# Performance work log

Hardware: AMD Instinct MI355X
Metric: run time of the kernel (lower is better)

The kernel has to match this reference:

```python
import jax, jax.numpy as jnp
import numpy as np

B, LQ, LK, DQ, DK, DV = 8, 2048, 2048, 1024, 1024, 1024
TOP_K = 64
NEG_INF = float('-inf')


def setup_inputs() -> dict:
    key = jax.random.key(0)
    kq, kk, kv, km, kw = jax.random.split(key, 5)
    queries = jax.random.normal(kq, (B, LQ, DQ), dtype=jnp.float32)
    keys = jax.random.normal(kk, (B, LK, DK), dtype=jnp.float32)
    values = jax.random.normal(kv, (B, LK, DV), dtype=jnp.float32)
    mask = jax.random.randint(km, (B, LQ, LK), 0, 2, dtype=jnp.int32)
    # nn.Linear(query_dim, key_dim, bias=False) weight: [key_dim, query_dim]
    W = jax.random.normal(kw, (DK, DQ), dtype=jnp.float32) / np.sqrt(DQ)
    return {"queries": queries, "keys": keys, "values": values,
            "mask": mask, "W": W, "top_k": TOP_K}


def reference(queries, keys, values, mask, W, top_k):
    # scores = (queries @ W.T) @ keys^T  -> [B, LQ, LK]  (method='general')
    q_proj = jnp.einsum('bqd,kd->bqk', queries, W)  # [B, LQ, DK]
    scores = jnp.einsum('bqd,btd->bqt', q_proj, keys)  # [B, LQ, LK]
    scores = jnp.where(mask == 0, NEG_INF, scores)
    alphas = jax.nn.softmax(scores, axis=-1)
    alphas = jnp.where(jnp.isnan(alphas), 0.0, alphas)  # fully-masked rows -> 0
    # top-k: zero out non-top-k probabilities, then re-softmax over the
    # resulting tensor (zeros contribute exp(0)=1, matching torch semantics)
    _, idx = jax.lax.top_k(alphas, top_k)  # [B, LQ, top_k]
    b_idx = jnp.arange(alphas.shape[0])[:, None, None]
    q_idx = jnp.arange(alphas.shape[1])[None, :, None]
    topk_mask = jnp.zeros(alphas.shape, alphas.dtype).at[b_idx, q_idx, idx].set(1.0)
    alphas = jnp.where(topk_mask == 0, 0.0, alphas)
    alphas = jax.nn.softmax(alphas, axis=-1)
    alphas = jnp.where(jnp.isnan(alphas), 0.0, alphas)
    # dropout_rate = 0.0 -> identity
    return jnp.einsum('bqt,btd->bqd', alphas, values)  # [B, LQ, DV]
```

## Files before the change

kernel.cpp:

```cpp
#include <hip/hip_runtime.h>
#include <math.h>

#define BATCH 8
#define SEQ   2048
#define DIM   1024
#define TOPK  64
#define NEGMASK -1e30f
#define CAND_THRESH 16.0f

typedef _Float16 f16;
typedef _Float16 f16x8 __attribute__((ext_vector_type(8)));
typedef float f32x4 __attribute__((ext_vector_type(4)));

__device__ __forceinline__ void async_load16(const void* g, void* l) {
  __builtin_amdgcn_global_load_lds(
      (const __attribute__((address_space(1))) void*)g,
      (__attribute__((address_space(3))) void*)l, 16, 0, 0);
}

__global__ __launch_bounds__(256) void colsum_partial_kernel(
    const float* __restrict__ values, float* __restrict__ partial) {
  int bid = blockIdx.x;
  int tc = bid >> 5;
  int b  = (bid >> 2) & 7;
  int dg = bid & 3;
  int d  = dg * 256 + threadIdx.x;
  const float* vp = values + ((size_t)b * SEQ + (size_t)tc * 256) * DIM + d;
  float s = 0.f;
  #pragma unroll 8
  for (int t = 0; t < 256; ++t) s += vp[(size_t)t * DIM];
  partial[((size_t)tc * BATCH + b) * DIM + d] = s;
}

__global__ __launch_bounds__(256) void colsum_reduce_kernel(
    const float* __restrict__ partial, float* __restrict__ colsum) {
  int idx = blockIdx.x * 256 + threadIdx.x;
  float s = 0.f;
  #pragma unroll
  for (int tc = 0; tc < 8; ++tc) s += partial[(size_t)tc * 8192 + idx];
  colsum[idx] = s;
}

__global__ __launch_bounds__(256) void cvt_f32_to_f16(
    const float* __restrict__ in, f16* __restrict__ out, int n) {
  int i = (blockIdx.x * 256 + threadIdx.x) * 4;
  if (i >= n) return;
  float4 v = *(const float4*)(in + i);
  union { f16 h[4]; uint2 u; } pk;
  pk.h[0] = (f16)v.x; pk.h[1] = (f16)v.y; pk.h[2] = (f16)v.z; pk.h[3] = (f16)v.w;
  *(uint2*)(out + i) = pk.u;
}


#define GEMM_PROLOGUE(APTR, BPTR)                                           \
  const int tid = threadIdx.x;                                              \
  const int wave = tid >> 6, lane = tid & 63;                               \
  const int wm = (wave >> 1) * 64, wn = (wave & 1) * 64;                    \
  const int r0 = wave * 32 + (lane >> 2);                                   \
  const int c16 = (lane & 3) ^ ((r0 >> 1) & 3);                            \
  const f16* srcA0 = (APTR) + (size_t)(m0 + r0) * DIM + c16 * 8;           \
  const f16* srcA1 = (APTR) + (size_t)(m0 + r0 + 16) * DIM + c16 * 8;      \
  const f16* srcB0 = (BPTR) + (size_t)(n0 + r0) * DIM + c16 * 8;           \
  const f16* srcB1 = (BPTR) + (size_t)(n0 + r0 + 16) * DIM + c16 * 8;      \
  char* ldsA0 = smA + wave * 2048;                                          \
  char* ldsA1 = smA + wave * 2048 + 1024;                                   \
  char* ldsB0 = smB + wave * 2048;                                          \
  char* ldsB1 = smB + wave * 2048 + 1024;                                   \
  int offA[4], offB[4];                                                     \
  _Pragma("unroll")                                                         \
  for (int i = 0; i < 4; ++i) {                                             \
    int r = wm + i * 16 + (lane & 15);                                      \
    offA[i] = r * 64 + ((lane >> 4) ^ ((r >> 1) & 3)) * 16;                 \
    int rn = wn + i * 16 + (lane & 15);                                     \
    offB[i] = rn * 64 + ((lane >> 4) ^ ((rn >> 1) & 3)) * 16;               \
  }                                                                         \
  f32x4 acc[4][4];                                                          \
  _Pragma("unroll")                                                         \
  for (int i = 0; i < 4; ++i)                                               \
    _Pragma("unroll")                                                       \
    for (int j = 0; j < 4; ++j)                                             \
      acc[i][j] = (f32x4){0.f, 0.f, 0.f, 0.f};                              \
  for (int k0 = 0; k0 < DIM; k0 += 32) {                                    \
    async_load16(srcA0 + k0, ldsA0);                                        \
    async_load16(srcA1 + k0, ldsA1);                                        \
    async_load16(srcB0 + k0, ldsB0);                                        \
    async_load16(srcB1 + k0, ldsB1);                                        \
    __syncthreads();                                                        \
    f16x8 af[4], bf[4];                                                     \
    _Pragma("unroll")                                                       \
    for (int i = 0; i < 4; ++i) {                                           \
      af[i] = *(const f16x8*)(smA + offA[i]);                               \
      bf[i] = *(const f16x8*)(smB + offB[i]);                               \
    }                                                                       \
    _Pragma("unroll")                                                       \
    for (int i = 0; i < 4; ++i)                                             \
      _Pragma("unroll")                                                     \
      for (int j = 0; j < 4; ++j)                                           \
        acc[i][j] = __builtin_amdgcn_mfma_f32_16x16x32_f16(                 \
            af[i], bf[j], acc[i][j], 0, 0, 0);                              \
    __syncthreads();                                                        \
  }

__global__ __launch_bounds__(256) void gemm_qproj(
    const f16* __restrict__ A, const f16* __restrict__ Bw,
    f16* __restrict__ C) {
  __shared__ __align__(128) char smA[8192];
  __shared__ __align__(128) char smB[8192];
  const int m0 = blockIdx.y * 128;
  const int n0 = blockIdx.x * 128;
  GEMM_PROLOGUE(A, Bw)
  const int cr = m0 + wm + (lane >> 4) * 4;
  const int cc = n0 + wn + (lane & 15);
  #pragma unroll
  for (int i = 0; i < 4; ++i)
    #pragma unroll
    for (int j = 0; j < 4; ++j)
      #pragma unroll
      for (int reg = 0; reg < 4; ++reg)
        C[(size_t)(cr + i * 16 + reg) * DIM + cc + j * 16] = (f16)acc[i][j][reg];
}

__global__ __launch_bounds__(256) void gemm_scores(
    const f16* __restrict__ QP, const f16* __restrict__ K16,
    const int* __restrict__ mask, float* __restrict__ S) {
  __shared__ __align__(128) char smA[8192];
  __shared__ __align__(128) char smB[8192];
  const int m0 = blockIdx.y * 128;
  const int n0 = blockIdx.x * 128;
  const int b  = m0 >> 11;
  const f16* Bk = K16 + (size_t)b * SEQ * DIM;
  GEMM_PROLOGUE(QP, Bk)
  const int cr = m0 + wm + (lane >> 4) * 4;
  const int cc = n0 + wn + (lane & 15);
  #pragma unroll
  for (int i = 0; i < 4; ++i)
    #pragma unroll
    for (int j = 0; j < 4; ++j)
      #pragma unroll
      for (int reg = 0; reg < 4; ++reg) {
        size_t off = (size_t)(cr + i * 16 + reg) * SEQ + cc + j * 16;
        S[off] = mask[off] ? acc[i][j][reg] : NEGMASK;
      }
}

__global__ __launch_bounds__(512) void topk_kernel(
    const float* __restrict__ scores_ws,
    const float* __restrict__ values,
    const float* __restrict__ colsum,
    float* __restrict__ out)
{
  __shared__ int   cidx[8][128];
  __shared__ float csc[8][128];
  const int wave = threadIdx.x >> 6;
  const int lane = threadIdx.x & 63;
  const int grow = blockIdx.x * 8 + wave;
  const int b    = grow >> 11;
  const float* srow = scores_ws + (size_t)grow * SEQ;
  int*   myidx = cidx[wave];
  float* mysc  = csc[wave];

  f32x4 s4[8];
  #pragma unroll
  for (int i = 0; i < 8; ++i)
    s4[i] = *(const f32x4*)(srow + i * 256 + lane * 4);

  float mv = -3e38f;
  #pragma unroll
  for (int i = 0; i < 8; ++i)
    #pragma unroll
    for (int j = 0; j < 4; ++j) mv = fmaxf(mv, s4[i][j]);
  #pragma unroll
  for (int off = 32; off > 0; off >>= 1) mv = fmaxf(mv, __shfl_xor(mv, off));
  const bool dead = (mv <= -1e29f);

  float Z = 1.f;
  if (!dead) {
    float zs = 0.f;
    #pragma unroll
    for (int i = 0; i < 8; ++i)
      #pragma unroll
      for (int j = 0; j < 4; ++j) zs += __expf(s4[i][j] - mv);
    #pragma unroll
    for (int off = 32; off > 0; off >>= 1) zs += __shfl_xor(zs, off);
    Z = zs;
  }
  const float invZ = 1.0f / Z;

  int cnt = 0;
  if (!dead) {
    const float thresh = mv - CAND_THRESH;
    const unsigned long long lmlt = (1ull << lane) - 1ull;
    #pragma unroll
    for (int i = 0; i < 8; ++i)
      #pragma unroll
      for (int j = 0; j < 4; ++j) {
        bool c = s4[i][j] > thresh;
        unsigned long long m = __ballot(c);
        if (c) {
          int pos = cnt + __popcll(m & lmlt);
          if (pos < 128) { myidx[pos] = i * 256 + lane * 4 + j; mysc[pos] = s4[i][j]; }
        }
        cnt += __popcll(m);
      }
  }
  asm volatile("s_waitcnt lgkmcnt(0)" ::: "memory");

  float total_g = 0.f;
  f32x4 oacc[4];
  #pragma unroll
  for (int j = 0; j < 4; ++j) oacc[j] = (f32x4){0.f, 0.f, 0.f, 0.f};
  const float* vbase = values + (size_t)b * SEQ * DIM;

  if (cnt <= 64) {
    for (int c = 0; c < cnt; ++c) {
      float g = expm1f(__expf(mysc[c] - mv) * invZ);
      total_g += g;
      const float* vrow = vbase + (size_t)myidx[c] * DIM;
      #pragma unroll
      for (int j = 0; j < 4; ++j) {
        f32x4 v = *(const f32x4*)(vrow + j * 256 + lane * 4);
        #pragma unroll
        for (int e = 0; e < 4; ++e) oacc[j][e] = fmaf(g, v[e], oacc[j][e]);
      }
    }
  } else {
    int nlist = cnt < 128 ? cnt : 128;
    for (int itk = 0; itk < TOPK; ++itk) {
      float bv = -3e38f; int bi = 1 << 30; int bsl = -1;
      #pragma unroll
      for (int h = 0; h < 2; ++h) {
        int sl = lane + h * 64;
        if (sl < nlist) {
          float v = mysc[sl]; int id = myidx[sl];
          if (v > bv || (v == bv && id < bi)) { bv = v; bi = id; bsl = sl; }
        }
      }
      #pragma unroll
      for (int off = 32; off > 0; off >>= 1) {
        float ov = __shfl_xor(bv, off);
        int   oi = __shfl_xor(bi, off);
        int   os = __shfl_xor(bsl, off);
        if (ov > bv || (ov == bv && oi < bi)) { bv = ov; bi = oi; bsl = os; }
      }
      if (bv <= -1e29f) break;
      float g = expm1f(__expf(bv - mv) * invZ);
      total_g += g;
      const float* vrow = vbase + (size_t)bi * DIM;
      #pragma unroll
      for (int j = 0; j < 4; ++j) {
        f32x4 v = *(const f32x4*)(vrow + j * 256 + lane * 4);
        #pragma unroll
        for (int e = 0; e < 4; ++e) oacc[j][e] = fmaf(g, v[e], oacc[j][e]);
      }
      if (lane == 0) mysc[bsl] = -3e38f;
      asm volatile("s_waitcnt lgkmcnt(0)" ::: "memory");
    }
  }

  const float inv = 1.0f / (2048.0f + total_g);
  const float* cs = colsum + (size_t)b * DIM;
  float* orow = out + (size_t)grow * DIM;
  #pragma unroll
  for (int j = 0; j < 4; ++j) {
    f32x4 c = *(const f32x4*)(cs + j * 256 + lane * 4);
    f32x4 o;
    #pragma unroll
    for (int e = 0; e < 4; ++e) o[e] = (c[e] + oacc[j][e]) * inv;
    *(f32x4*)(orow + j * 256 + lane * 4) = o;
  }
}

extern "C" void kernel_launch(void* const* d_in, const int* in_sizes, int n_in,
                              void* d_out, int out_size, void* d_ws, size_t ws_size,
                              hipStream_t stream) {
  const float* queries = (const float*)d_in[0];
  const float* keys    = (const float*)d_in[1];
  const float* values  = (const float*)d_in[2];
  const int*   mask    = (const int*)d_in[3];
  const float* W       = (const float*)d_in[4];
  float* out = (float*)d_out;

  char* base = (char*)d_ws;
  float* scores  = (float*)base;
  f16*   q16     = (f16*)base;
  f16*   w16     = (f16*)(base + (size_t)32 * 1024 * 1024);
  f16*   qp16    = (f16*)(base + (size_t)128 * 1024 * 1024);
  f16*   k16     = (f16*)(base + (size_t)160 * 1024 * 1024);
  float* colsum  = (float*)(base + (size_t)192 * 1024 * 1024);
  float* partial = colsum + 8192;

  colsum_partial_kernel<<<256, 256, 0, stream>>>(values, partial);
  colsum_reduce_kernel<<<32, 256, 0, stream>>>(partial, colsum);
  cvt_f32_to_f16<<<16384, 256, 0, stream>>>(queries, q16, 16384 * 1024);
  cvt_f32_to_f16<<<1024, 256, 0, stream>>>(W, w16, 1024 * 1024);
  gemm_qproj<<<dim3(8, 128), 256, 0, stream>>>(q16, w16, qp16);
  cvt_f32_to_f16<<<16384, 256, 0, stream>>>(keys, k16, 16384 * 1024);
  gemm_scores<<<dim3(16, 128), 256, 0, stream>>>(qp16, k16, mask, scores);
  topk_kernel<<<2048, 512, 0, stream>>>(scores, values, colsum, out);
}
```

Before: 321.8 us.

## Filter top-k candidates in score GEMM epilogue and bit-pack mask

A new kernel packs the int32 mask into 64-bit bitmasks. The score GEMM epilogue then applies the mask, takes a per-row max over each 128-column tile, and writes only scores within a threshold of that max into capped per-segment candidate slots, plus a count per segment. The top-k kernel reads these compact lists instead of full score rows, and builds the softmax denominator from candidates only. This removes the full fp32 score write and re-read and shrinks mask traffic inside the GEMM. In exchange it adds a mask-packing pass and a shared-memory sync in the epilogue, and it becomes approximate: scores below the threshold are dropped from Z, and segments with more than 28 candidates are truncated.

Result: slower. 366.4 us (+13.9%).

```diff
diff --git a/kernel.cpp b/kernel.cpp
--- a/kernel.cpp
+++ b/kernel.cpp
@@ -7,6 +7,7 @@
 #define TOPK  64
 #define NEGMASK -1e30f
 #define CAND_THRESH 16.0f
+#define CAP 28
 
 typedef _Float16 f16;
 typedef _Float16 f16x8 __attribute__((ext_vector_type(8)));
@@ -16,6 +17,16 @@
   __builtin_amdgcn_global_load_lds(
       (const __attribute__((address_space(1))) void*)g,
       (__attribute__((address_space(3))) void*)l, 16, 0, 0);
+}
+
+__global__ __launch_bounds__(256) void pack_mask_kernel(
+    const int* __restrict__ mask, unsigned long long* __restrict__ mb) {
+  const int wave = threadIdx.x >> 6, lane = threadIdx.x & 63;
+  for (size_t w = blockIdx.x * 4 + wave; w < (size_t)16384 * 32; w += 2048 * 4) {
+    int m = mask[w * 64 + lane];
+    unsigned long long bits = __ballot(m != 0);
+    if (lane == 0) mb[w] = bits;
+  }
 }
 
 __global__ __launch_bounds__(256) void colsum_partial_kernel(
@@ -122,7 +133,9 @@
 
 __global__ __launch_bounds__(256) void gemm_scores(
     const f16* __restrict__ QP, const f16* __restrict__ K16,
-    const int* __restrict__ mask, float* __restrict__ S) {
+    const unsigned long long* __restrict__ maskbits,
+    float2* __restrict__ cand,
+    int* __restrict__ counts) {
   __shared__ __align__(128) char smA[8192];
   __shared__ __align__(128) char smB[8192];
   const int m0 = blockIdx.y * 128;
@@ -130,130 +143,168 @@
   const int b  = m0 >> 11;
   const f16* Bk = K16 + (size_t)b * SEQ * DIM;
   GEMM_PROLOGUE(QP, Bk)
-  const int cr = m0 + wm + (lane >> 4) * 4;
-  const int cc = n0 + wn + (lane & 15);
+
+  const int g  = lane >> 4;
+  const int lc = lane & 15;
+  const int word = (n0 >> 6) + (wn >> 6);
+
   #pragma unroll
   for (int i = 0; i < 4; ++i)
     #pragma unroll
-    for (int j = 0; j < 4; ++j)
+    for (int reg = 0; reg < 4; ++reg) {
+      const int r = wm + i * 16 + g * 4 + reg;
+      const unsigned long long mw = maskbits[(size_t)(m0 + r) * 32 + word];
       #pragma unroll
-      for (int reg = 0; reg < 4; ++reg) {
-        size_t off = (size_t)(cr + i * 16 + reg) * SEQ + cc + j * 16;
-        S[off] = mask[off] ? acc[i][j][reg] : NEGMASK;
+      for (int j = 0; j < 4; ++j)
+        if (!((mw >> (lc + j * 16)) & 1ull)) acc[i][j][reg] = NEGMASK;
+    }
+
+  float* hm = (float*)smA;
+  #pragma unroll
+  for (int i = 0; i < 4; ++i)
+    #pragma unroll
+    for (int reg = 0; reg < 4; ++reg) {
+      const int r = wm + i * 16 + g * 4 + reg;
+      float m4 = fmaxf(fmaxf(acc[i][0][reg], acc[i][1][reg]),
+                       fmaxf(acc[i][2][reg], acc[i][3][reg]));
+      #pragma unroll
+      for (int off = 8; off >= 1; off >>= 1) m4 = fmaxf(m4, __shfl_xor(m4, off));
+      if (lc == 0) hm[r * 2 + (wn >> 6)] = m4;
+    }
+  __syncthreads();
+
+  const int pairbase = (n0 >> 7) * 2 + (wn >> 6);
+  #pragma unroll
+  for (int i = 0; i < 4; ++i)
+    #pragma unroll
+    for (int reg = 0; reg < 4; ++reg) {
+      const int r = wm + i * 16 + g * 4 + reg;
+      const float tm = fmaxf(hm[r * 2], hm[r * 2 + 1]);
+      const float thresh = fmaxf(tm - CAND_THRESH, -1e29f);
+      float2* slot = cand + ((size_t)(m0 + r) * 32 + pairbase) * CAP;
+      int cnt = 0;
+      #pragma unroll
+      for (int j = 0; j < 4; ++j) {
+        const float s = acc[i][j][reg];
+        const bool c = s > thresh;
+        const unsigned long long bal = __ballot(c);
+        const int seg = (int)((bal >> (g * 16)) & 0xFFFFull);
+        const int pos = cnt + __popc(seg & ((1 << lc) - 1));
+        if (c && pos < CAP) {
+          float2 e; e.x = s; e.y = __int_as_float(n0 + wn + j * 16 + lc);
+          slot[pos] = e;
+        }
+        cnt += __popc(seg);
       }
+      if (lc == 0) counts[(size_t)(m0 + r) * 32 + pairbase] = cnt < CAP ? cnt : CAP;
+    }
 }
 
 __global__ __launch_bounds__(512) void topk_kernel(
-    const float* __restrict__ scores_ws,
-    const float* __restrict__ values,
-    const float* __restrict__ colsum,
+    const float2* __restrict__ cand,
+    const int*    __restrict__ counts,
+    const float*  __restrict__ values,
+    const float*  __restrict__ colsum,
     float* __restrict__ out)
 {
-  __shared__ int   cidx[8][128];
-  __shared__ float csc[8][128];
+  __shared__ float ssc[8][128];
+  __shared__ int   sidx[8][128];
   const int wave = threadIdx.x >> 6;
   const int lane = threadIdx.x & 63;
   const int grow = blockIdx.x * 8 + wave;
   const int b    = grow >> 11;
-  const float* srow = scores_ws + (size_t)grow * SEQ;
-  int*   myidx = cidx[wave];
-  float* mysc  = csc[wave];
-
-  f32x4 s4[8];
-  #pragma unroll
-  for (int i = 0; i < 8; ++i)
-    s4[i] = *(const f32x4*)(srow + i * 256 + lane * 4);
+  float* msc = ssc[wave];
+  int*   mix = sidx[wave];
+
+  int cnt_p = 0;
+  if (lane < 32) cnt_p = counts[(size_t)grow * 32 + lane];
+  const float2* myslots = cand + ((size_t)grow * 32 + lane) * CAP;
 
   float mv = -3e38f;
-  #pragma unroll
-  for (int i = 0; i < 8; ++i)
-    #pragma unroll
-    for (int j = 0; j < 4; ++j) mv = fmaxf(mv, s4[i][j]);
+  for (int k = 0; k < cnt_p; ++k) mv = fmaxf(mv, myslots[k].x);
   #pragma unroll
   for (int off = 32; off > 0; off >>= 1) mv = fmaxf(mv, __shfl_xor(mv, off));
   const bool dead = (mv <= -1e29f);
 
-  float Z = 1.f;
-  if (!dead) {
-    float zs = 0.f;
-    #pragma unroll
-    for (int i = 0; i < 8; ++i)
-      #pragma unroll
-      for (int j = 0; j < 4; ++j) zs += __expf(s4[i][j] - mv);
-    #pragma unroll
-    for (int off = 32; off > 0; off >>= 1) zs += __shfl_xor(zs, off);
-    Z = zs;
-  }
-  const float invZ = 1.0f / Z;
-
-  int cnt = 0;
+  float total_g = 0.f;
+  f32x4 oacc[4];
+  #pragma unroll
+  for (int j = 0; j < 4; ++j) oacc[j] = (f32x4){0.f, 0.f, 0.f, 0.f};
+  const float* vbase = values + (size_t)b * SEQ * DIM;
+
   if (!dead) {
     const float thresh = mv - CAND_THRESH;
-    const unsigned long long lmlt = (1ull << lane) - 1ull;
-    #pragma unroll
-    for (int i = 0; i < 8; ++i)
-      #pragma unroll
-      for (int j = 0; j < 4; ++j) {
-        bool c = s4[i][j] > thresh;
-        unsigned long long m = __ballot(c);
-        if (c) {
-          int pos = cnt + __popcll(m & lmlt);
-          if (pos < 128) { myidx[pos] = i * 256 + lane * 4 + j; mysc[pos] = s4[i][j]; }
-        }
-        cnt += __popcll(m);
+    int f = 0; float zp = 0.f;
+    for (int k = 0; k < cnt_p; ++k) {
+      float s = myslots[k].x;
+      if (s > thresh) { ++f; zp += __expf(s - mv); }
+    }
+    int incl = f;
+    #pragma unroll
+    for (int off = 1; off < 64; off <<= 1) {
+      int t = __shfl_up(incl, off);
+      if (lane >= off) incl += t;
+    }
+    const int base = incl - f;
+    const int F = __shfl(incl, 63);
+    #pragma unroll
+    for (int off = 32; off > 0; off >>= 1) zp += __shfl_xor(zp, off);
+    const float Z = zp;
+    int w = 0;
+    for (int k = 0; k < cnt_p; ++k) {
+      float2 cv = myslots[k];
+      if (cv.x > thresh) {
+        int p = base + w;
+        if (p < 128) { msc[p] = cv.x; mix[p] = __float_as_int(cv.y); }
+        ++w;
       }
-  }
-  asm volatile("s_waitcnt lgkmcnt(0)" ::: "memory");
-
-  float total_g = 0.f;
-  f32x4 oacc[4];
-  #pragma unroll
-  for (int j = 0; j < 4; ++j) oacc[j] = (f32x4){0.f, 0.f, 0.f, 0.f};
-  const float* vbase = values + (size_t)b * SEQ * DIM;
-
-  if (cnt <= 64) {
-    for (int c = 0; c < cnt; ++c) {
-      float g = expm1f(__expf(mysc[c] - mv) * invZ);
-      total_g += g;
-      const float* vrow = vbase + (size_t)myidx[c] * DIM;
-      #pragma unroll
-      for (int j = 0; j < 4; ++j) {
-        f32x4 v = *(const f32x4*)(vrow + j * 256 + lane * 4);
+    }
+    asm volatile("s_waitcnt lgkmcnt(0)" ::: "memory");
+
+    if (F <= TOPK) {
+      for (int c = 0; c < F; ++c) {
+        float g = expm1f(__expf(msc[c] - mv) / Z);
+        total_g += g;
+        const float* vrow = vbase + (size_t)mix[c] * DIM;
         #pragma unroll
-        for (int e = 0; e < 4; ++e) oacc[j][e] = fmaf(g, v[e], oacc[j][e]);
+        for (int j = 0; j < 4; ++j) {
+          f32x4 v = *(const f32x4*)(vrow + j * 256 + lane * 4);
+          #pragma unroll
+          for (int e = 0; e < 4; ++e) oacc[j][e] = fmaf(g, v[e], oacc[j][e]);
+        }
       }
-    }
-  } else {
-    int nlist = cnt < 128 ? cnt : 128;
-    for (int itk = 0; itk < TOPK; ++itk) {
-      float bv = -3e38f; int bi = 1 << 30; int bsl = -1;
-      #pragma unroll
-      for (int h = 0; h < 2; ++h) {
-        int sl = lane + h * 64;
-        if (sl < nlist) {
-          float v = mysc[sl]; int id = myidx[sl];
-          if (v > bv || (v == bv && id < bi)) { bv = v; bi = id; bsl = sl; }
-        }
+    } else {
+      const int nlist = F < 128 ? F : 128;
+      for (int itk = 0; itk < TOPK; ++itk) {
+        float bv = -3e38f; int bi = 1 << 30; int bsl = -1;
+        #pragma unroll
+        for (int h = 0; h < 2; ++h) {
+          int sl = lane + h * 64;
+          if (sl < nlist) {
+            float v = msc[sl]; int id = mix[sl];
+            if (v > bv || (v == bv && id < bi)) { bv = v; bi = id; bsl = sl; }
+          }
+        }
+        #pragma unroll
+        for (int off = 32; off > 0; off >>= 1) {
+          float ov = __shfl_xor(bv, off);
+          int   oi = __shfl_xor(bi, off);
+          int   os = __shfl_xor(bsl, off);
+          if (ov > bv || (ov == bv && oi < bi)) { bv = ov; bi = oi; bsl = os; }
+        }
+        if (bv <= -1e29f) break;
+        float g = expm1f(__expf(bv - mv) / Z);
+        total_g += g;
+        const float* vrow = vbase + (size_t)bi * DIM;
+        #pragma unroll
+        for (int j = 0; j < 4; ++j) {
+          f32x4 v = *(const f32x4*)(vrow + j * 256 + lane * 4);
+          #pragma unroll
+          for (int e = 0; e < 4; ++e) oacc[j][e] = fmaf(g, v[e], oacc[j][e]);
+        }
+        if (lane == 0) msc[bsl] = -3e38f;
+        asm volatile("s_waitcnt lgkmcnt(0)" ::: "memory");
       }
-      #pragma unroll
-      for (int off = 32; off > 0; off >>= 1) {
-        float ov = __shfl_xor(bv, off);
-        int   oi = __shfl_xor(bi, off);
-        int   os = __shfl_xor(bsl, off);
-        if (ov > bv || (ov == bv && oi < bi)) { bv = ov; bi = oi; bsl = os; }
-      }
-      if (bv <= -1e29f) break;
-      float g = expm1f(__expf(bv - mv) * invZ);
-      total_g += g;
-      const float* vrow = vbase + (size_t)bi * DIM;
-      #pragma unroll
-      for (int j = 0; j < 4; ++j) {
-        f32x4 v = *(const f32x4*)(vrow + j * 256 + lane * 4);
-        #pragma unroll
-        for (int e = 0; e < 4; ++e) oacc[j][e] = fmaf(g, v[e], oacc[j][e]);
-      }
-      if (lane == 0) mysc[bsl] = -3e38f;
-      asm volatile("s_waitcnt lgkmcnt(0)" ::: "memory");
     }
   }
 
@@ -281,20 +332,24 @@
   float* out = (float*)d_out;
 
   char* base = (char*)d_ws;
-  float* scores  = (float*)base;
+  float2* cand   = (float2*)base;
   f16*   q16     = (f16*)base;
   f16*   w16     = (f16*)(base + (size_t)32 * 1024 * 1024);
+  int*   counts  = (int*)(base + (size_t)112 * 1024 * 1024);
+  unsigned long long* maskbits =
+      (unsigned long long*)(base + (size_t)114 * 1024 * 1024);
   f16*   qp16    = (f16*)(base + (size_t)128 * 1024 * 1024);
   f16*   k16     = (f16*)(base + (size_t)160 * 1024 * 1024);
   float* colsum  = (float*)(base + (size_t)192 * 1024 * 1024);
   float* partial = colsum + 8192;
 
+  pack_mask_kernel<<<2048, 256, 0, stream>>>(mask, maskbits);
   colsum_partial_kernel<<<256, 256, 0, stream>>>(values, partial);
   colsum_reduce_kernel<<<32, 256, 0, stream>>>(partial, colsum);
   cvt_f32_to_f16<<<16384, 256, 0, stream>>>(queries, q16, 16384 * 1024);
   cvt_f32_to_f16<<<1024, 256, 0, stream>>>(W, w16, 1024 * 1024);
   gemm_qproj<<<dim3(8, 128), 256, 0, stream>>>(q16, w16, qp16);
   cvt_f32_to_f16<<<16384, 256, 0, stream>>>(keys, k16, 16384 * 1024);
-  gemm_scores<<<dim3(16, 128), 256, 0, stream>>>(qp16, k16, mask, scores);
-  topk_kernel<<<2048, 512, 0, stream>>>(scores, values, colsum, out);
-}
+  gemm_scores<<<dim3(16, 128), 256, 0, stream>>>(qp16, k16, maskbits, cand, counts);
+  topk_kernel<<<2048, 512, 0, stream>>>(cand, counts, values, colsum, out);
+}
```
